# Kernel optimization log

Measured on AMD Instinct MI355X. Metric: run time of the kernel, lower is better.

Reference implementation:

```python
import jax, jax.numpy as jnp
import numpy as np

B, S, D, FD = 2, 2048, 1024, 4096
EPS_LN = 1e-5


def _l2norm(x):
    n = jnp.linalg.norm(x, axis=-1, keepdims=True)
    return x / jnp.maximum(n, 1e-12)


def _layernorm(x, w, b):
    m = x.mean(-1, keepdims=True)
    v = ((x - m) ** 2).mean(-1, keepdims=True)
    return (x - m) / jnp.sqrt(v + EPS_LN) * w + b


def _spl(x, mu_w, mu_b, gate, proto):
    # cosine-similarity gated linear (SparseProtoLinear)
    scores = _l2norm(x) @ _l2norm(proto).T          # [..., out]
    rw = jax.nn.relu(scores - gate)
    comp = x @ mu_w.T + mu_b
    return comp * rw


def _rotate_half(x):
    h = x.shape[-1] // 2
    return jnp.concatenate([-x[..., h:], x[..., :h]], axis=-1)


def _forward(x, cos, sin,
             ln1_w, ln1_b, ln2_w, ln2_b,
             qkv_mu, qkv_proto, qkv_bias, qkv_gate,
             o_mu, o_proto, o_bias, o_gate,
             f1_mu, f1_proto, f1_bias, f1_gate,
             f2_mu, f2_proto, f2_bias, f2_gate,
             pt_qkv, pt_o, pt_f1, pt_f2,
             pln_qkv_w, pln_qkv_b, pln_o_w, pln_o_b,
             pln_f1_w, pln_f1_b, pln_f2_w, pln_f2_b,
             prev_qkv, prev_o, prev_f1, prev_f2):
    # effective protos: proto_weight + LN(Linear(prev_proto))
    eff_qkv = qkv_proto + _layernorm(prev_qkv @ pt_qkv.T, pln_qkv_w, pln_qkv_b)
    eff_o   = o_proto   + _layernorm(prev_o   @ pt_o.T,   pln_o_w,   pln_o_b)
    eff_f1  = f1_proto  + _layernorm(prev_f1  @ pt_f1.T,  pln_f1_w,  pln_f1_b)
    eff_f2  = f2_proto  + _layernorm(prev_f2  @ pt_f2.T,  pln_f2_w,  pln_f2_b)

    # attention
    attn_in = _layernorm(x, ln1_w, ln1_b)
    m_qkv = _spl(attn_in, qkv_mu, qkv_bias, qkv_gate, eff_qkv)   # [B,S,3D]
    q, k, v = jnp.split(m_qkv, 3, axis=-1)
    c = cos[None]; s = sin[None]
    q = q * c + _rotate_half(q) * s
    k = k * c + _rotate_half(k) * s
    scale = 1.0 / jnp.sqrt(jnp.asarray(D, x.dtype))
    scores = jnp.einsum('bqd,bkd->bqk', q, k) * scale            # [B,S,S]
    causal = jnp.tril(jnp.ones((S, S), dtype=bool))
    scores = jnp.where(causal[None], scores, jnp.finfo(x.dtype).min)
    attn = jax.nn.softmax(scores, axis=-1)
    attn_out = jnp.einsum('bqk,bkd->bqd', attn, v)
    m_o = _spl(attn_out, o_mu, o_bias, o_gate, eff_o)
    x1 = x + m_o

    # ffn (DynamicInfiniteExpert)
    ffn_in = _layernorm(x1, ln2_w, ln2_b)
    m1 = _spl(ffn_in, f1_mu, f1_bias, f1_gate, eff_f1)           # [B,S,FD]
    h = jax.nn.relu(m1)
    m2 = _spl(h, f2_mu, f2_bias, f2_gate, eff_f2)                # [B,S,D]
    return x1 + m2


def setup_inputs() -> dict:
    key = jax.random.key(0)
    ks = iter(jax.random.split(key, 64))

    def nrm(shape, scale=1.0):
        return jax.random.normal(next(ks), shape, dtype=jnp.float32) * scale

    # RoPE tables
    pos = np.arange(S, dtype=np.float32)
    inv_freq = 1.0 / (10000.0 ** (np.arange(0, D, 2, dtype=np.float32) / D))
    freqs = np.outer(pos, inv_freq)
    emb = np.concatenate([freqs, freqs], axis=-1)
    cos = jnp.asarray(np.cos(emb)); sin = jnp.asarray(np.sin(emb))

    sD = 1.0 / np.sqrt(D); sF = 1.0 / np.sqrt(FD)
    inp = {
        'x': nrm((B, S, D)), 'cos': cos, 'sin': sin,
        'ln1_w': jnp.ones((D,)), 'ln1_b': jnp.zeros((D,)),
        'ln2_w': jnp.ones((D,)), 'ln2_b': jnp.zeros((D,)),
        'qkv_mu': nrm((3 * D, D), sD), 'qkv_proto': nrm((3 * D, D), sD),
        'qkv_bias': jnp.zeros((3 * D,)), 'qkv_gate': jnp.zeros((3 * D,)),
        'o_mu': nrm((D, D), sD), 'o_proto': nrm((D, D), sD),
        'o_bias': jnp.zeros((D,)), 'o_gate': jnp.zeros((D,)),
        'f1_mu': nrm((FD, D), sD), 'f1_proto': nrm((FD, D), sD),
        'f1_bias': jnp.zeros((FD,)), 'f1_gate': jnp.zeros((FD,)),
        'f2_mu': nrm((D, FD), sF), 'f2_proto': nrm((D, FD), sF),
        'f2_bias': jnp.zeros((D,)), 'f2_gate': jnp.zeros((D,)),
        'pt_qkv': nrm((D, D), sD), 'pt_o': nrm((D, D), sD),
        'pt_f1': nrm((D, D), sD), 'pt_f2': nrm((FD, FD), sF),
        'pln_qkv_w': jnp.ones((D,)), 'pln_qkv_b': jnp.zeros((D,)),
        'pln_o_w': jnp.ones((D,)), 'pln_o_b': jnp.zeros((D,)),
        'pln_f1_w': jnp.ones((D,)), 'pln_f1_b': jnp.zeros((D,)),
        'pln_f2_w': jnp.ones((FD,)), 'pln_f2_b': jnp.zeros((FD,)),
        'prev_qkv': nrm((3 * D, D), sD), 'prev_o': nrm((D, D), sD),
        'prev_f1': nrm((FD, D), sD), 'prev_f2': nrm((D, FD), sF),
    }
    return inp


def reference(x, cos, sin,
              ln1_w, ln1_b, ln2_w, ln2_b,
              qkv_mu, qkv_proto, qkv_bias, qkv_gate,
              o_mu, o_proto, o_bias, o_gate,
              f1_mu, f1_proto, f1_bias, f1_gate,
              f2_mu, f2_proto, f2_bias, f2_gate,
              pt_qkv, pt_o, pt_f1, pt_f2,
              pln_qkv_w, pln_qkv_b, pln_o_w, pln_o_b,
              pln_f1_w, pln_f1_b, pln_f2_w, pln_f2_b,
              prev_qkv, prev_o, prev_f1, prev_f2):
    return _forward(x, cos, sin, ln1_w, ln1_b, ln2_w, ln2_b,
                    qkv_mu, qkv_proto, qkv_bias, qkv_gate,
                    o_mu, o_proto, o_bias, o_gate,
                    f1_mu, f1_proto, f1_bias, f1_gate,
                    f2_mu, f2_proto, f2_bias, f2_gate,
                    pt_qkv, pt_o, pt_f1, pt_f2,
                    pln_qkv_w, pln_qkv_b, pln_o_w, pln_o_b,
                    pln_f1_w, pln_f1_b, pln_f2_w, pln_f2_b,
                    prev_qkv, prev_o, prev_f1, prev_f2)
```

## Files before the change

### kernel.cpp

```cpp
#include <hip/hip_runtime.h>
#include <cstdint>

typedef unsigned short u16;
typedef __attribute__((ext_vector_type(8))) short sh8;
typedef __attribute__((ext_vector_type(4))) float f32x4;

struct __align__(8) us4 { u16 x, y, z, w; };

__device__ __forceinline__ u16 f2bf(float f) {
  unsigned u = __float_as_uint(f);
  u += 0x7FFFu + ((u >> 16) & 1u);
  return (u16)(u >> 16);
}
__device__ __forceinline__ float bf2f(u16 h) {
  return __uint_as_float((unsigned)h << 16);
}

__device__ __forceinline__ float blk_sum(float v, float* red) {
#pragma unroll
  for (int o = 32; o; o >>= 1) v += __shfl_xor(v, o);
  __syncthreads();
  if ((threadIdx.x & 63) == 0) red[threadIdx.x >> 6] = v;
  __syncthreads();
  return red[0] + red[1] + red[2] + red[3];
}
__device__ __forceinline__ float blk_max(float v, float* red) {
#pragma unroll
  for (int o = 32; o; o >>= 1) v = fmaxf(v, __shfl_xor(v, o));
  __syncthreads();
  if ((threadIdx.x & 63) == 0) red[threadIdx.x >> 6] = v;
  __syncthreads();
  return fmaxf(fmaxf(red[0], red[1]), fmaxf(red[2], red[3]));
}

__global__ void cvt_bf16(const float* __restrict__ S, u16* __restrict__ D, long n4) {
  long i = (long)blockIdx.x * blockDim.x + threadIdx.x;
  if (i >= n4) return;
  float4 v = ((const float4*)S)[i];
  us4 o; o.x = f2bf(v.x); o.y = f2bf(v.y); o.z = f2bf(v.z); o.w = f2bf(v.w);
  ((us4*)D)[i] = o;
}

__global__ void fillv(float* __restrict__ o, long n, float v) {
  long i = (long)blockIdx.x * blockDim.x + threadIdx.x;
  if (i < n) o[i] = v;
}

#define GL16(gp, lp)                                                        \
  __builtin_amdgcn_global_load_lds(                                         \
      (const __attribute__((address_space(1))) void*)(gp),                  \
      (__attribute__((address_space(3))) void*)(lp), 16, 0, 0)

template <typename CT>
__global__ __launch_bounds__(512, 1) void gemm256(
    const u16* __restrict__ A, const u16* __restrict__ B, CT* __restrict__ C,
    int M, int N, int K, int lda, int ldb, int kchunk) {
  extern __shared__ u16 lds[];
  int tid = threadIdx.x;
  int wid = tid >> 6, lane = tid & 63;
  int wm = wid >> 2, wn = wid & 3;
  int bm = blockIdx.x, bn = blockIdx.y;
  int k0s = 0, nt;
  if (kchunk) {
    k0s = blockIdx.z * kchunk;
    C += (size_t)blockIdx.z * M * (size_t)N;
    nt = kchunk >> 5;
  } else {
    nt = K >> 5;
  }
  const size_t baseArow = (size_t)bm * 256;
  const size_t baseBrow = (size_t)bn * 256;

  int ci = (wid << 6) + lane;
  int rowS = ci >> 2;
  int kcS = (ci ^ (ci >> 3)) & 3;
  const u16* gA0 = A + (baseArow + rowS) * lda + k0s + kcS * 8;
  const u16* gA1 = gA0 + (size_t)128 * lda;
  const u16* gB0 = B + (baseBrow + rowS) * ldb + k0s + kcS * 8;
  const u16* gB1 = gB0 + (size_t)128 * ldb;
  u16* dBase = lds + (wid << 9);

  int l15 = lane & 15, l4 = lane >> 4;
  int aoff[8], boff[4];
#pragma unroll
  for (int fr = 0; fr < 8; ++fr) {
    int by = (wm * 128 + fr * 16 + l15) * 64 + l4 * 16;
    aoff[fr] = (by ^ (((by >> 7) & 3) << 4)) >> 1;
  }
#pragma unroll
  for (int fc = 0; fc < 4; ++fc) {
    int by = (wn * 64 + fc * 16 + l15) * 64 + l4 * 16;
    boff[fc] = 8192 + ((by ^ (((by >> 7) & 3) << 4)) >> 1);
  }

  f32x4 acc[8][4];
  const f32x4 zf = {0.f, 0.f, 0.f, 0.f};
#pragma unroll
  for (int i = 0; i < 8; ++i)
#pragma unroll
    for (int j = 0; j < 4; ++j) acc[i][j] = zf;

#define STAGE256(ts)                                                  \
  do {                                                                \
    int ss_ = (ts) & 3;                                               \
    int kk_ = (ts) << 5;                                              \
    u16* d_ = dBase + ss_ * 16384;                                    \
    GL16(gA0 + kk_, d_);                                              \
    GL16(gA1 + kk_, d_ + 4096);                                       \
    GL16(gB0 + kk_, d_ + 8192);                                       \
    GL16(gB1 + kk_, d_ + 12288);                                      \
  } while (0)

  STAGE256(0);
  STAGE256(1);
  STAGE256(2);
  asm volatile("s_waitcnt vmcnt(8)" ::: "memory");
  __builtin_amdgcn_s_barrier();
  __builtin_amdgcn_sched_barrier(0);

  for (int t = 0; t < nt; ++t) {
    int ts = t + 3;
    if (ts < nt) STAGE256(ts);

    const u16* sl = lds + (t & 3) * 16384;
    sh8 af[8], bfv[4];
#pragma unroll
    for (int fc = 0; fc < 4; ++fc) bfv[fc] = *(const sh8*)(sl + boff[fc]);
#pragma unroll
    for (int fr = 0; fr < 8; ++fr) af[fr] = *(const sh8*)(sl + aoff[fr]);

    __builtin_amdgcn_s_setprio(1);
#pragma unroll
    for (int fr = 0; fr < 8; ++fr)
#pragma unroll
      for (int fc = 0; fc < 4; ++fc)
        acc[fr][fc] = __builtin_amdgcn_mfma_f32_16x16x32_bf16(af[fr], bfv[fc],
                                                              acc[fr][fc], 0, 0, 0);
    __builtin_amdgcn_s_setprio(0);

    int rem = nt - 2 - t;
    if (rem >= 2)      asm volatile("s_waitcnt vmcnt(8)" ::: "memory");
    else if (rem == 1) asm volatile("s_waitcnt vmcnt(4)" ::: "memory");
    else if (rem == 0) asm volatile("s_waitcnt vmcnt(0)" ::: "memory");
    if (t < nt - 1) {
      __builtin_amdgcn_s_barrier();
      __builtin_amdgcn_sched_barrier(0);
    }
  }
#undef STAGE256

  int cr = l4 << 2, cc = l15;
  const size_t rbase = baseArow + wm * 128 + cr;
  const size_t cbase = baseBrow + wn * 64 + cc;
#pragma unroll
  for (int fr = 0; fr < 8; ++fr)
#pragma unroll
    for (int fc = 0; fc < 4; ++fc) {
      size_t cb = (rbase + fr * 16) * (size_t)N + cbase + fc * 16;
#pragma unroll
      for (int r = 0; r < 4; ++r) {
        float v = acc[fr][fc][r];
        if constexpr (sizeof(CT) == 2) C[cb + (size_t)r * N] = (CT)f2bf(v);
        else                           C[cb + (size_t)r * N] = v;
      }
    }
}

template <typename CT>
__global__ __launch_bounds__(256, 2) void gemm_bt(
    const u16* __restrict__ A, const u16* __restrict__ B, CT* __restrict__ C,
    int M, int N, int K, int lda, int ldb,
    int mode, long zsA, long zsB, long zsC) {
  int bm, bn;
  int z = blockIdx.z;
  if (mode == 3) {
    int t = blockIdx.x;
    int m = (int)floorf((sqrtf(8.f * t + 1.f) - 1.f) * 0.5f);
    while ((m + 1) * (m + 2) / 2 <= t) ++m;
    while (m * (m + 1) / 2 > t) --m;
    bm = m; bn = t - m * (m + 1) / 2;
  } else {
    bm = blockIdx.x; bn = blockIdx.y;
  }
  int k0s = 0, k0e = K;
  if (mode == 1) {
    int kc = K / gridDim.z;
    k0s = z * kc; k0e = k0s + kc;
    C += (size_t)z * M * (size_t)N;
  } else if (mode == 2 || mode == 3) {
    A += (size_t)z * zsA; B += (size_t)z * zsB; C += (size_t)z * zsC;
  } else if (mode == 4) {
    A += (size_t)z * zsA; B += (size_t)z * zsB; C += (size_t)z * zsC;
    k0e = (bm + 1) * 128;
  } else if (mode == 5) {
    int Mz = (int)((zsB >> (z * 16)) & 0xFFFF);
    if (bm * 128 >= Mz) return;
    A += (size_t)z * zsA; B += (size_t)z * 1048576; C += (size_t)z * zsC;
  }

  __shared__ __align__(16) u16 As[128 * 32];
  __shared__ __align__(16) u16 Bs[128 * 32];
  int tid = threadIdx.x, wid = tid >> 6, lane = tid & 63;
  int wr = (wid >> 1) << 6, wc = (wid & 1) << 6;
  int lr = lane & 15, lk = (lane >> 4) << 3;

  f32x4 acc[4][4];
  const f32x4 zf = {0.f, 0.f, 0.f, 0.f};
#pragma unroll
  for (int i = 0; i < 4; ++i)
#pragma unroll
    for (int j = 0; j < 4; ++j) acc[i][j] = zf;

  int r0 = tid >> 2, c0 = (tid & 3) << 3;
  const size_t baseA = (size_t)bm * 128, baseB = (size_t)bn * 128;
  const u16* Ab = A + baseA * lda;
  const u16* Bp = B + baseB * ldb;

  for (int k0 = k0s; k0 < k0e; k0 += 32) {
    GL16(Ab + (size_t)r0 * lda + k0 + c0, As + (wid << 9));
    GL16(Ab + (size_t)(64 + r0) * lda + k0 + c0, As + 2048 + (wid << 9));
    GL16(Bp + (size_t)r0 * ldb + k0 + c0, Bs + (wid << 9));
    GL16(Bp + (size_t)(64 + r0) * ldb + k0 + c0, Bs + 2048 + (wid << 9));
    __syncthreads();
    sh8 af[4], bfr[4];
#pragma unroll
    for (int f = 0; f < 4; ++f) {
      af[f]  = *(const sh8*)(As + (wr + f * 16 + lr) * 32 + lk);
      bfr[f] = *(const sh8*)(Bs + (wc + f * 16 + lr) * 32 + lk);
    }
#pragma unroll
    for (int i = 0; i < 4; ++i)
#pragma unroll
      for (int j = 0; j < 4; ++j)
        acc[i][j] = __builtin_amdgcn_mfma_f32_16x16x32_bf16(af[i], bfr[j], acc[i][j], 0, 0, 0);
    __syncthreads();
  }

  int cr = (lane >> 4) << 2, cc = lane & 15;
#pragma unroll
  for (int i = 0; i < 4; ++i)
#pragma unroll
    for (int j = 0; j < 4; ++j) {
      size_t cb = (baseA + wr + i * 16 + cr) * (size_t)N + (baseB + wc + j * 16 + cc);
#pragma unroll
      for (int r = 0; r < 4; ++r) {
        float v = acc[i][j][r];
        if constexpr (sizeof(CT) == 2) C[cb + (size_t)r * N] = (CT)f2bf(v);
        else                           C[cb + (size_t)r * N] = v;
      }
    }
}

__global__ void ln_rows(const float* __restrict__ X, const float* __restrict__ w,
                        const float* __restrict__ b, u16* __restrict__ Y,
                        float* __restrict__ norms, int C) {
  __shared__ float red[4];
  int row = blockIdx.x;
  const float* x = X + (size_t)row * C;
  int nv = C >> 2;
  float s = 0.f, ss = 0.f;
  for (int i = threadIdx.x; i < nv; i += 256) {
    float4 v = ((const float4*)x)[i];
    s += v.x + v.y + v.z + v.w;
    ss += v.x * v.x + v.y * v.y + v.z * v.z + v.w * v.w;
  }
  s = blk_sum(s, red);
  ss = blk_sum(ss, red);
  float mean = s / C;
  float inv = rsqrtf(fmaxf(ss / C - mean * mean, 0.f) + 1e-5f);
  float nrm = 0.f;
  for (int i = threadIdx.x; i < nv; i += 256) {
    float4 v = ((const float4*)x)[i];
    float4 wv = ((const float4*)w)[i];
    float4 bv = ((const float4*)b)[i];
    float y0 = (v.x - mean) * inv * wv.x + bv.x;
    float y1 = (v.y - mean) * inv * wv.y + bv.y;
    float y2 = (v.z - mean) * inv * wv.z + bv.z;
    float y3 = (v.w - mean) * inv * wv.w + bv.w;
    nrm += y0 * y0 + y1 * y1 + y2 * y2 + y3 * y3;
    us4 o; o.x = f2bf(y0); o.y = f2bf(y1); o.z = f2bf(y2); o.w = f2bf(y3);
    ((us4*)(Y + (size_t)row * C))[i] = o;
  }
  nrm = blk_sum(nrm, red);
  if (threadIdx.x == 0) norms[row] = fmaxf(sqrtf(nrm), 1e-12f);
}

__global__ void ln_add_norm(const u16* __restrict__ T0, const u16* __restrict__ T1,
                            const float* __restrict__ P,
                            const float* __restrict__ w, const float* __restrict__ b,
                            u16* __restrict__ E, float* __restrict__ norms, int C) {
  __shared__ float red[4];
  int row = blockIdx.x;
  const us4* t0 = (const us4*)(T0 + (size_t)row * C);
  const us4* t1 = T1 ? (const us4*)(T1 + (size_t)row * C) : nullptr;
  const float* p = P + (size_t)row * C;
  int nv = C >> 2;
  float s = 0.f, ss = 0.f;
  for (int i = threadIdx.x; i < nv; i += 256) {
    us4 v = t0[i];
    float f0 = bf2f(v.x), f1 = bf2f(v.y), f2 = bf2f(v.z), f3 = bf2f(v.w);
    if (t1) {
      us4 v1 = t1[i];
      f0 += bf2f(v1.x); f1 += bf2f(v1.y); f2 += bf2f(v1.z); f3 += bf2f(v1.w);
    }
    s += f0 + f1 + f2 + f3;
    ss += f0 * f0 + f1 * f1 + f2 * f2 + f3 * f3;
  }
  s = blk_sum(s, red);
  ss = blk_sum(ss, red);
  float mean = s / C;
  float inv = rsqrtf(fmaxf(ss / C - mean * mean, 0.f) + 1e-5f);
  float nrm = 0.f;
  for (int i = threadIdx.x; i < nv; i += 256) {
    us4 v = t0[i];
    float f0 = bf2f(v.x), f1 = bf2f(v.y), f2 = bf2f(v.z), f3 = bf2f(v.w);
    if (t1) {
      us4 v1 = t1[i];
      f0 += bf2f(v1.x); f1 += bf2f(v1.y); f2 += bf2f(v1.z); f3 += bf2f(v1.w);
    }
    float4 pv = ((const float4*)p)[i];
    float4 wv = ((const float4*)w)[i];
    float4 bv = ((const float4*)b)[i];
    float y0 = pv.x + (f0 - mean) * inv * wv.x + bv.x;
    float y1 = pv.y + (f1 - mean) * inv * wv.y + bv.y;
    float y2 = pv.z + (f2 - mean) * inv * wv.z + bv.z;
    float y3 = pv.w + (f3 - mean) * inv * wv.w + bv.w;
    nrm += y0 * y0 + y1 * y1 + y2 * y2 + y3 * y3;
    us4 o; o.x = f2bf(y0); o.y = f2bf(y1); o.z = f2bf(y2); o.w = f2bf(y3);
    ((us4*)(E + (size_t)row * C))[i] = o;
  }
  nrm = blk_sum(nrm, red);
  if (threadIdx.x == 0) norms[row] = fmaxf(sqrtf(nrm), 1e-12f);
}

__global__ void rownorm_bf(const u16* __restrict__ X, float* __restrict__ norms, int C) {
  __shared__ float red[4];
  int row = blockIdx.x;
  const us4* x = (const us4*)(X + (size_t)row * C);
  int nv = C >> 2;
  float nrm = 0.f;
  for (int i = threadIdx.x; i < nv; i += 256) {
    us4 v = x[i];
    float a = bf2f(v.x), b = bf2f(v.y), c = bf2f(v.z), d = bf2f(v.w);
    nrm += a * a + b * b + c * c + d * d;
  }
  nrm = blk_sum(nrm, red);
  if (threadIdx.x == 0) norms[row] = fmaxf(sqrtf(nrm), 1e-12f);
}

__device__ __forceinline__ void epi4(const u16* gr, int C, int c, float rr,
                                     const float* bias, const float* gate,
                                     const float* cn, float* o) {
  us4 cv = *(const us4*)(gr + c);
  us4 dv = *(const us4*)(gr + C + c);
  float4 bv = *(const float4*)(bias + c);
  float4 gv = *(const float4*)(gate + c);
  float4 nv = *(const float4*)(cn + c);
  float cf[4] = {bf2f(cv.x), bf2f(cv.y), bf2f(cv.z), bf2f(cv.w)};
  float df[4] = {bf2f(dv.x), bf2f(dv.y), bf2f(dv.z), bf2f(dv.w)};
  float bb[4] = {bv.x, bv.y, bv.z, bv.w};
  float gg[4] = {gv.x, gv.y, gv.z, gv.w};
  float nn[4] = {nv.x, nv.y, nv.z, nv.w};
#pragma unroll
  for (int j = 0; j < 4; ++j) {
    float sc = df[j] / (rr * nn[j]);
    o[j] = (cf[j] + bb[j]) * fmaxf(sc - gg[j], 0.f);
  }
}

__global__ void spl_rope_row(const u16* __restrict__ G, const float* __restrict__ bias,
                             const float* __restrict__ gate, const float* __restrict__ rn,
                             const float* __restrict__ cn, const float* __restrict__ CT_,
                             const float* __restrict__ ST_, u16* __restrict__ MQ) {
  int r = blockIdx.x;
  int s = r & 2047;
  const u16* gr = G + (size_t)r * 6144;
  u16* outr = MQ + (size_t)r * 3072;
  float rr = rn[r];
  int t = threadIdx.x;

  int qk = (t >> 7);
  int c = qk * 1024 + ((t & 127) << 2);
  int d = c - qk * 1024;
  float a0[4], a1[4];
  epi4(gr, 3072, c, rr, bias, gate, cn, a0);
  epi4(gr, 3072, c + 512, rr, bias, gate, cn, a1);
  const float* ct = CT_ + (size_t)s * 1024;
  const float* st = ST_ + (size_t)s * 1024;
  float4 c0 = *(const float4*)(ct + d);
  float4 s0 = *(const float4*)(st + d);
  float4 c1 = *(const float4*)(ct + d + 512);
  float4 s1 = *(const float4*)(st + d + 512);
  float cc0[4] = {c0.x, c0.y, c0.z, c0.w}, ss0[4] = {s0.x, s0.y, s0.z, s0.w};
  float cc1[4] = {c1.x, c1.y, c1.z, c1.w}, ss1[4] = {s1.x, s1.y, s1.z, s1.w};
  us4 o0, o1;
  o0.x = f2bf(a0[0] * cc0[0] - a1[0] * ss0[0]);
  o0.y = f2bf(a0[1] * cc0[1] - a1[1] * ss0[1]);
  o0.z = f2bf(a0[2] * cc0[2] - a1[2] * ss0[2]);
  o0.w = f2bf(a0[3] * cc0[3] - a1[3] * ss0[3]);
  o1.x = f2bf(a1[0] * cc1[0] + a0[0] * ss1[0]);
  o1.y = f2bf(a1[1] * cc1[1] + a0[1] * ss1[1]);
  o1.z = f2bf(a1[2] * cc1[2] + a0[2] * ss1[2]);
  o1.w = f2bf(a1[3] * cc1[3] + a0[3] * ss1[3]);
  *(us4*)(outr + c) = o0;
  *(us4*)(outr + c + 512) = o1;

  int cv_ = 2048 + (t << 2);
  float vv[4];
  epi4(gr, 3072, cv_, rr, bias, gate, cn, vv);
  us4 ov; ov.x = f2bf(vv[0]); ov.y = f2bf(vv[1]); ov.z = f2bf(vv[2]); ov.w = f2bf(vv[3]);
  *(us4*)(outr + cv_) = ov;
}

__global__ void spl_f1_row(const u16* __restrict__ G, const float* __restrict__ bias,
                           const float* __restrict__ gate, const float* __restrict__ rn,
                           const float* __restrict__ cn, u16* __restrict__ H,
                           float* __restrict__ rn_h) {
  __shared__ float red[4];
  int r = blockIdx.x;
  const u16* gr = G + (size_t)r * 8192;
  u16* hr = H + (size_t)r * 4096;
  float rr = rn[r];
  float nrm = 0.f;
  for (int c = threadIdx.x << 2; c < 4096; c += 1024) {
    float o[4];
    epi4(gr, 4096, c, rr, bias, gate, cn, o);
#pragma unroll
    for (int j = 0; j < 4; ++j) {
      o[j] = fmaxf(o[j], 0.f);
      nrm += o[j] * o[j];
    }
    us4 ov; ov.x = f2bf(o[0]); ov.y = f2bf(o[1]); ov.z = f2bf(o[2]); ov.w = f2bf(o[3]);
    *(us4*)(hr + c) = ov;
  }
  nrm = blk_sum(nrm, red);
  if (threadIdx.x == 0) rn_h[r] = fmaxf(sqrtf(nrm), 1e-12f);
}

__global__ void spl_o_ln_row(const u16* __restrict__ G, const float* __restrict__ bias,
                             const float* __restrict__ gate, const float* __restrict__ rn,
                             const float* __restrict__ cn, const float* __restrict__ xres,
                             const float* __restrict__ lw, const float* __restrict__ lb,
                             float* __restrict__ X1, u16* __restrict__ Y,
                             float* __restrict__ rn_ffn) {
  __shared__ float red[4];
  int r = blockIdx.x;
  int c = threadIdx.x << 2;
  const u16* gr = G + (size_t)r * 2048;
  float o[4];
  epi4(gr, 1024, c, rn[r], bias, gate, cn, o);
  float4 rv = *(const float4*)(xres + (size_t)r * 1024 + c);
  o[0] += rv.x; o[1] += rv.y; o[2] += rv.z; o[3] += rv.w;
  float4 xo = {o[0], o[1], o[2], o[3]};
  *(float4*)(X1 + (size_t)r * 1024 + c) = xo;
  float s = o[0] + o[1] + o[2] + o[3];
  float ss = o[0] * o[0] + o[1] * o[1] + o[2] * o[2] + o[3] * o[3];
  s = blk_sum(s, red);
  ss = blk_sum(ss, red);
  float mean = s * (1.f / 1024.f);
  float inv = rsqrtf(fmaxf(ss * (1.f / 1024.f) - mean * mean, 0.f) + 1e-5f);
  float4 wv = *(const float4*)(lw + c);
  float4 bv = *(const float4*)(lb + c);
  float ww[4] = {wv.x, wv.y, wv.z, wv.w}, bb[4] = {bv.x, bv.y, bv.z, bv.w};
  float nrm = 0.f;
  us4 ov;
  u16* op = (u16*)&ov;
#pragma unroll
  for (int j = 0; j < 4; ++j) {
    float y = (o[j] - mean) * inv * ww[j] + bb[j];
    nrm += y * y;
    op[j] = f2bf(y);
  }
  *(us4*)(Y + (size_t)r * 1024 + c) = ov;
  nrm = blk_sum(nrm, red);
  if (threadIdx.x == 0) rn_ffn[r] = fmaxf(sqrtf(nrm), 1e-12f);
}

__global__ void spl_epi_p(const u16* __restrict__ G0, const u16* __restrict__ G1,
                          const float* __restrict__ bias, const float* __restrict__ gate,
                          const float* __restrict__ rn, const float* __restrict__ cn,
                          const float* __restrict__ resid, float* __restrict__ out) {
  int r = blockIdx.x;
  int c = threadIdx.x << 2;
  size_t rowb = (size_t)r * 2048;
  us4 c0 = *(const us4*)(G0 + rowb + c);
  us4 c1 = *(const us4*)(G1 + rowb + c);
  us4 d0 = *(const us4*)(G0 + rowb + 1024 + c);
  us4 d1 = *(const us4*)(G1 + rowb + 1024 + c);
  float4 bv = *(const float4*)(bias + c);
  float4 gv = *(const float4*)(gate + c);
  float4 nv = *(const float4*)(cn + c);
  float4 rv = *(const float4*)(resid + (size_t)r * 1024 + c);
  float rr = rn[r];
  float cf[4] = {bf2f(c0.x) + bf2f(c1.x), bf2f(c0.y) + bf2f(c1.y),
                 bf2f(c0.z) + bf2f(c1.z), bf2f(c0.w) + bf2f(c1.w)};
  float df[4] = {bf2f(d0.x) + bf2f(d1.x), bf2f(d0.y) + bf2f(d1.y),
                 bf2f(d0.z) + bf2f(d1.z), bf2f(d0.w) + bf2f(d1.w)};
  float bb[4] = {bv.x, bv.y, bv.z, bv.w};
  float gg[4] = {gv.x, gv.y, gv.z, gv.w};
  float nn[4] = {nv.x, nv.y, nv.z, nv.w};
  float re[4] = {rv.x, rv.y, rv.z, rv.w};
  float4 ov;
  float* op = (float*)&ov;
#pragma unroll
  for (int j = 0; j < 4; ++j) {
    float sc = df[j] / (rr * nn[j]);
    op[j] = (cf[j] + bb[j]) * fmaxf(sc - gg[j], 0.f) + re[j];
  }
  *(float4*)(out + (size_t)r * 1024 + c) = ov;
}

__global__ void vtrans(const u16* __restrict__ MQ, u16* __restrict__ VT) {
  __shared__ u16 tile[32][33];
  int b = blockIdx.z;
  int s0 = blockIdx.x << 5, d0 = blockIdx.y << 5;
  int tx = threadIdx.x, ty = threadIdx.y;
  for (int r = ty; r < 32; r += 8)
    tile[r][tx] = MQ[((size_t)(b * 2048 + s0 + r)) * 3072 + 2048 + d0 + tx];
  __syncthreads();
  for (int r = ty; r < 32; r += 8)
    VT[(size_t)b * 1024 * 2048 + (size_t)(d0 + r) * 2048 + s0 + tx] = tile[tx][r];
}

__global__ void softmax_causal(const float* __restrict__ S, u16* __restrict__ P) {
  __shared__ float red[4];
  int b = blockIdx.x >> 11;
  int q = blockIdx.x & 2047;
  const float* row = S + ((size_t)b << 22) + (size_t)q * 2048;
  u16* prow = P + ((size_t)b << 22) + (size_t)q * 2048;
  int nv = q + 1;
  int wcap = ((q >> 7) + 1) << 7;
  int base = threadIdx.x * 8;
  float e[8];
  float m = -3.4e38f;
  float xv[8];
  bool live = base < nv;
  if (live) {
    float4 a = *(const float4*)(row + base);
    float4 bq = *(const float4*)(row + base + 4);
    xv[0] = a.x; xv[1] = a.y; xv[2] = a.z; xv[3] = a.w;
    xv[4] = bq.x; xv[5] = bq.y; xv[6] = bq.z; xv[7] = bq.w;
#pragma unroll
    for (int j = 0; j < 8; ++j) {
      xv[j] *= 0.03125f;
      if (base + j < nv) m = fmaxf(m, xv[j]);
    }
  }
  m = blk_max(m, red);
  float ssum = 0.f;
#pragma unroll
  for (int j = 0; j < 8; ++j) {
    e[j] = (live && base + j < nv) ? __expf(xv[j] - m) : 0.f;
    ssum += e[j];
  }
  ssum = blk_sum(ssum, red);
  float invs = 1.f / ssum;
  if (base < wcap) {
    us4 o;
    o.x = f2bf(e[0] * invs); o.y = f2bf(e[1] * invs);
    o.z = f2bf(e[2] * invs); o.w = f2bf(e[3] * invs);
    ((us4*)prow)[threadIdx.x * 2] = o;
    o.x = f2bf(e[4] * invs); o.y = f2bf(e[5] * invs);
    o.z = f2bf(e[6] * invs); o.w = f2bf(e[7] * invs);
    ((us4*)prow)[threadIdx.x * 2 + 1] = o;
  }
}

extern "C" void kernel_launch(void* const* d_in, const int* in_sizes, int n_in,
                              void* d_out, int out_size, void* d_ws, size_t ws_size,
                              hipStream_t stream) {
  (void)in_sizes;
  const float* x         = (const float*)d_in[0];
  const float* cosT      = (const float*)d_in[1];
  const float* sinT      = (const float*)d_in[2];
  const float* ln1_w     = (const float*)d_in[3];
  const float* ln1_b     = (const float*)d_in[4];
  const float* ln2_w     = (const float*)d_in[5];
  const float* ln2_b     = (const float*)d_in[6];
  const float* qkv_mu    = (const float*)d_in[7];
  const float* qkv_proto = (const float*)d_in[8];
  const float* qkv_bias  = (const float*)d_in[9];
  const float* qkv_gate  = (const float*)d_in[10];
  const float* o_mu      = (const float*)d_in[11];
  const float* o_proto   = (const float*)d_in[12];
  const float* o_bias    = (const float*)d_in[13];
  const float* o_gate    = (const float*)d_in[14];
  const float* f1_mu     = (const float*)d_in[15];
  const float* f1_proto  = (const float*)d_in[16];
  const float* f1_bias   = (const float*)d_in[17];
  const float* f1_gate   = (const float*)d_in[18];
  const float* f2_mu     = (const float*)d_in[19];
  const float* f2_proto  = (const float*)d_in[20];
  const float* f2_bias   = (const float*)d_in[21];
  const float* f2_gate   = (const float*)d_in[22];
  const float* pt_qkv    = (const float*)d_in[23];
  const float* pt_o      = (const float*)d_in[24];
  const float* pt_f1     = (const float*)d_in[25];
  const float* pt_f2     = (const float*)d_in[26];
  const float* pln_qkv_w = (const float*)d_in[27];
  const float* pln_qkv_b = (const float*)d_in[28];
  const float* pln_o_w   = (const float*)d_in[29];
  const float* pln_o_b   = (const float*)d_in[30];
  const float* pln_f1_w  = (const float*)d_in[31];
  const float* pln_f1_b  = (const float*)d_in[32];
  const float* pln_f2_w  = (const float*)d_in[33];
  const float* pln_f2_b  = (const float*)d_in[34];
  const float* prev_qkv  = (const float*)d_in[35];
  const float* prev_o    = (const float*)d_in[36];
  const float* prev_f1   = (const float*)d_in[37];
  const float* prev_f2   = (const float*)d_in[38];

  const long D = 1024, TD = 3072, FD = 4096, R = 4096;

  char* W = (char*)d_ws;
  size_t off = 0;
  auto alloc = [&](size_t bytes) {
    void* p = W + off;
    off = (off + bytes + 255) & ~(size_t)255;
    return p;
  };
  char* GOUT = (char*)alloc(67108864);
  u16*  RC   = (u16*)alloc(33554432);
  u16*  wq   = (u16*)alloc(2 * TD * D * 2);
  u16*  wo   = (u16*)alloc(2 * D * D * 2);
  u16*  wf1  = (u16*)alloc(2 * FD * D * 2);
  u16*  wf2  = (u16*)alloc(2 * D * FD * 2);
  float* X1  = (float*)alloc(R * D * 4);
  u16*  P1   = (u16*)alloc(R * D * 2);
  u16*  VT   = (u16*)alloc(2 * D * 2048 * 2);
  u16*  AOB  = (u16*)alloc(R * D * 2);
  float* pnq     = (float*)alloc(TD * 4);
  float* pno     = (float*)alloc(D * 4);
  float* pnf1    = (float*)alloc(FD * 4);
  float* pnf2    = (float*)alloc(D * 4);
  float* rn_ain  = (float*)alloc(R * 4);
  float* rn_aout = (float*)alloc(R * 4);
  float* rn_ffn  = (float*)alloc(R * 4);
  float* rn_h    = (float*)alloc(R * 4);
  size_t need = off;

  if (n_in < 39 || need > ws_size) {
    long n = out_size;
    fillv<<<dim3((unsigned)((n + 255) / 256)), 256, 0, stream>>>((float*)d_out, n, 12345.0f);
    return;
  }

  u16* SA = (u16*)GOUT;
  u16* SB = (u16*)(GOUT + 25165824);
  float* SCORES = (float*)GOUT;
  u16* PB = (u16*)(GOUT + 33554432);

  auto cvt = [&](const float* s, u16* d, long n) {
    long n4 = n >> 2;
    cvt_bf16<<<dim3((unsigned)((n4 + 255) / 256)), 256, 0, stream>>>(s, d, n4);
  };

  cvt(prev_f1,  SA,            FD * D);
  cvt(prev_qkv, SA + 4194304,  TD * D);
  cvt(prev_o,   SA + 8388608,  D * D);
  cvt(pt_f1,    SB,            D * D);
  cvt(pt_qkv,   SB + 1048576,  D * D);
  cvt(pt_o,     SB + 2097152,  D * D);
  {
    long Mz = 4096L | (3072L << 16) | (1024L << 32);
    gemm_bt<u16><<<dim3(32, 8, 3), 256, 0, stream>>>(
        SA, SB, RC, 4096, 1024, 1024, 1024, 1024, 5, 4194304, Mz, 4194304);
  }
  ln_add_norm<<<4096, 256, 0, stream>>>(RC, nullptr, f1_proto, pln_f1_w, pln_f1_b,
                                        wf1 + (size_t)FD * D, pnf1, 1024);
  ln_add_norm<<<3072, 256, 0, stream>>>(RC + 4194304, nullptr, qkv_proto, pln_qkv_w,
                                        pln_qkv_b, wq + (size_t)TD * D, pnq, 1024);
  ln_add_norm<<<1024, 256, 0, stream>>>(RC + 8388608, nullptr, o_proto, pln_o_w,
                                        pln_o_b, wo + (size_t)D * D, pno, 1024);
  cvt(prev_f2, SA, D * FD);
  cvt(pt_f2,   SB, (long)FD * FD);
  gemm_bt<u16><<<dim3(8, 32, 2), 256, 0, stream>>>(
      SA, SB, RC, 1024, 4096, 4096, 4096, 4096, 1, 0, 0, 0);
  ln_add_norm<<<1024, 256, 0, stream>>>(RC, RC + 4194304, f2_proto, pln_f2_w, pln_f2_b,
                                        wf2 + (size_t)D * FD, pnf2, 4096);
  cvt(qkv_mu, wq, TD * D);
  cvt(o_mu,   wo, D * D);
  cvt(f1_mu,  wf1, FD * D);
  cvt(f2_mu,  wf2, D * FD);

  ln_rows<<<4096, 256, 0, stream>>>(x, ln1_w, ln1_b, P1, rn_ain, 1024);
  gemm256<u16><<<dim3(16, 24), 512, 131072, stream>>>(
      P1, wq, (u16*)GOUT, 4096, 6144, 1024, 1024, 1024, 0);
  spl_rope_row<<<4096, 256, 0, stream>>>(
      (u16*)GOUT, qkv_bias, qkv_gate, rn_ain, pnq, cosT, sinT, RC);

  vtrans<<<dim3(64, 32, 2), dim3(32, 8), 0, stream>>>(RC, VT);
  gemm_bt<float><<<dim3(136, 1, 2), 256, 0, stream>>>(
      RC, RC + 1024, SCORES, 2048, 2048, 1024, 3072, 3072,
      3, 2048L * 3072, 2048L * 3072, 1L << 22);
  softmax_causal<<<4096, 256, 0, stream>>>(SCORES, PB);
  gemm_bt<u16><<<dim3(16, 8, 2), 256, 0, stream>>>(
      PB, VT, AOB, 2048, 1024, 2048, 2048, 2048,
      4, 1L << 22, 1024L * 2048, 2048L * 1024);
  rownorm_bf<<<4096, 256, 0, stream>>>(AOB, rn_aout, 1024);

  gemm_bt<u16><<<dim3(32, 16, 1), 256, 0, stream>>>(
      AOB, wo, (u16*)GOUT, 4096, 2048, 1024, 1024, 1024, 0, 0, 0, 0);
  spl_o_ln_row<<<4096, 256, 0, stream>>>(
      (u16*)GOUT, o_bias, o_gate, rn_aout, pno, x, ln2_w, ln2_b, X1, P1, rn_ffn);

  gemm256<u16><<<dim3(16, 32), 512, 131072, stream>>>(
      P1, wf1, (u16*)GOUT, 4096, 8192, 1024, 1024, 1024, 0);
  spl_f1_row<<<4096, 256, 0, stream>>>(
      (u16*)GOUT, f1_bias, f1_gate, rn_ffn, pnf1, RC, rn_h);
  gemm256<u16><<<dim3(16, 8, 2), 512, 131072, stream>>>(
      RC, wf2, (u16*)GOUT, 4096, 2048, 4096, 4096, 4096, 2048);
  spl_epi_p<<<4096, 256, 0, stream>>>(
      (u16*)GOUT, (u16*)GOUT + 8388608, f2_bias, f2_gate, rn_h, pnf2,
      X1, (float*)d_out);
}
```

Before: 589.7 us.

## Interleave global-to-LDS loads with MFMA quadrants in 256-tile GEMM main loop

```diff
diff --git a/kernel.cpp b/kernel.cpp
--- a/kernel.cpp
+++ b/kernel.cpp
@@ -120,23 +120,75 @@
 
   for (int t = 0; t < nt; ++t) {
     int ts = t + 3;
-    if (ts < nt) STAGE256(ts);
-
+    bool st = ts < nt;
+    int ss_ = ts & 3, kk_ = ts << 5;
+    u16* d_ = dBase + ss_ * 16384;
     const u16* sl = lds + (t & 3) * 16384;
+
     sh8 af[8], bfv[4];
-#pragma unroll
-    for (int fc = 0; fc < 4; ++fc) bfv[fc] = *(const sh8*)(sl + boff[fc]);
-#pragma unroll
-    for (int fr = 0; fr < 8; ++fr) af[fr] = *(const sh8*)(sl + aoff[fr]);
-
+
+    if (st) GL16(gA0 + kk_, d_);
+#pragma unroll
+    for (int fr = 0; fr < 4; ++fr) af[fr] = *(const sh8*)(sl + aoff[fr]);
+#pragma unroll
+    for (int fc = 0; fc < 2; ++fc) bfv[fc] = *(const sh8*)(sl + boff[fc]);
+    __builtin_amdgcn_s_barrier();
+    __builtin_amdgcn_sched_barrier(0);
     __builtin_amdgcn_s_setprio(1);
 #pragma unroll
-    for (int fr = 0; fr < 8; ++fr)
-#pragma unroll
-      for (int fc = 0; fc < 4; ++fc)
+    for (int fr = 0; fr < 4; ++fr)
+#pragma unroll
+      for (int fc = 0; fc < 2; ++fc)
         acc[fr][fc] = __builtin_amdgcn_mfma_f32_16x16x32_bf16(af[fr], bfv[fc],
                                                               acc[fr][fc], 0, 0, 0);
     __builtin_amdgcn_s_setprio(0);
+    __builtin_amdgcn_sched_barrier(0);
+    __builtin_amdgcn_s_barrier();
+
+    if (st) GL16(gA1 + kk_, d_ + 4096);
+#pragma unroll
+    for (int fc = 2; fc < 4; ++fc) bfv[fc] = *(const sh8*)(sl + boff[fc]);
+    __builtin_amdgcn_s_barrier();
+    __builtin_amdgcn_sched_barrier(0);
+    __builtin_amdgcn_s_setprio(1);
+#pragma unroll
+    for (int fr = 0; fr < 4; ++fr)
+#pragma unroll
+      for (int fc = 2; fc < 4; ++fc)
+        acc[fr][fc] = __builtin_amdgcn_mfma_f32_16x16x32_bf16(af[fr], bfv[fc],
+                                                              acc[fr][fc], 0, 0, 0);
+    __builtin_amdgcn_s_setprio(0);
+    __builtin_amdgcn_sched_barrier(0);
+    __builtin_amdgcn_s_barrier();
+
+    if (st) GL16(gB0 + kk_, d_ + 8192);
+#pragma unroll
+    for (int fr = 4; fr < 8; ++fr) af[fr] = *(const sh8*)(sl + aoff[fr]);
+    __builtin_amdgcn_s_barrier();
+    __builtin_amdgcn_sched_barrier(0);
+    __builtin_amdgcn_s_setprio(1);
+#pragma unroll
+    for (int fr = 4; fr < 8; ++fr)
+#pragma unroll
+      for (int fc = 2; fc < 4; ++fc)
+        acc[fr][fc] = __builtin_amdgcn_mfma_f32_16x16x32_bf16(af[fr], bfv[fc],
+                                                              acc[fr][fc], 0, 0, 0);
+    __builtin_amdgcn_s_setprio(0);
+    __builtin_amdgcn_sched_barrier(0);
+    __builtin_amdgcn_s_barrier();
+
+    if (st) GL16(gB1 + kk_, d_ + 12288);
+    __builtin_amdgcn_s_barrier();
+    __builtin_amdgcn_sched_barrier(0);
+    __builtin_amdgcn_s_setprio(1);
+#pragma unroll
+    for (int fr = 4; fr < 8; ++fr)
+#pragma unroll
+      for (int fc = 0; fc < 2; ++fc)
+        acc[fr][fc] = __builtin_amdgcn_mfma_f32_16x16x32_bf16(af[fr], bfv[fc],
+                                                              acc[fr][fc], 0, 0, 0);
+    __builtin_amdgcn_s_setprio(0);
+    __builtin_amdgcn_sched_barrier(0);
 
     int rem = nt - 2 - t;
     if (rem >= 2)      asm volatile("s_waitcnt vmcnt(8)" ::: "memory");
```

Result: slower. 603.9 us (+2.4%).
